# Performance work log

Measured on AMD Instinct MI355X. Metric: run time of the kernel, lower is better.

## Reference

```python
import jax, jax.numpy as jnp
import numpy as np

IN_FEATURES = 4096
OUT_FEATURES = 4096
ALPHA = 0.002
BETA = 0.01


def setup_inputs() -> dict:
    key = jax.random.key(0)
    k_x, k_w, k_b = jax.random.split(key, 3)
    # int8 activations, weights, bias (matching torch.randint(-127, 127, ...))
    x = jax.random.randint(k_x, (4, 2048, IN_FEATURES), -127, 127, dtype=jnp.int32).astype(jnp.int8)
    weight = jax.random.randint(k_w, (OUT_FEATURES, IN_FEATURES), -127, 127, dtype=jnp.int32).astype(jnp.int8)
    bias = jax.random.randint(k_b, (1, OUT_FEATURES), -127, 127, dtype=jnp.int32).astype(jnp.int8)
    a = jnp.float32(ALPHA)
    b = jnp.float32(BETA)
    return {"x": x, "weight": weight, "bias": bias, "a": a, "b": b}


def reference(x, weight, bias, a, b):
    # int8 bias add, and requantize-to-int8 epilogue.
    x_shape = x.shape
    x2d = x.reshape(-1, x_shape[-1])                       # [M, K] int8
    # int32 accumulation: acc = x @ W^T
    acc = jnp.matmul(x2d.astype(jnp.int32), weight.T.astype(jnp.int32),
                     preferred_element_type=jnp.int32)      # [M, N] int32
    # epilogue: alpha * acc + beta * bias, round + clamp to int8 range
    y = a * acc.astype(jnp.float32) + b * bias.astype(jnp.float32)
    y = jnp.clip(jnp.round(y), -128.0, 127.0).astype(jnp.int8)
    return y.reshape(*x_shape[:-1], -1)
```

## Files before the change

### kernel.cpp

```cpp
#include <hip/hip_runtime.h>

#define K_DIM 4096
#define N_DIM 4096
#define NT (K_DIM / 128)

typedef int v4i __attribute__((ext_vector_type(4)));
typedef int v16i __attribute__((ext_vector_type(16)));

__device__ __forceinline__ void gload_lds16(const void* g, void* l) {
  __builtin_amdgcn_global_load_lds(
      (const __attribute__((address_space(1))) void*)g,
      (__attribute__((address_space(3))) void*)l, 16, 0, 0);
}

__device__ __forceinline__ int pack4(int4 w) {
  return (w.x & 0xff) | ((w.y & 0xff) << 8) | ((w.z & 0xff) << 16) | (w.w << 24);
}

__global__ __launch_bounds__(256) void pack_kernel(const int* __restrict__ src,
                                                   int4* __restrict__ dst, int n16) {
  int i = blockIdx.x * 256 + threadIdx.x;
  if (i >= n16) return;
  const int4* s = (const int4*)src + (size_t)i * 4;
  int4 w0 = s[0], w1 = s[1], w2 = s[2], w3 = s[3];
  int4 r;
  r.x = pack4(w0); r.y = pack4(w1); r.z = pack4(w2); r.w = pack4(w3);
  dst[i] = r;
}

__global__ __launch_bounds__(512, 2) void gemm256(
    const char* __restrict__ Ap, const char* __restrict__ Bp,
    const int* __restrict__ bias, const float* __restrict__ pa,
    const float* __restrict__ pb, int* __restrict__ out) {
  extern __shared__ __align__(16) char lds[];

  const int tid = threadIdx.x;
  const int wid = tid >> 6;
  const int lane = tid & 63;

  const int nwg = gridDim.x;
  const int cpx = nwg >> 3;
  const int flat = blockIdx.x;
  const int wg = (flat & 7) * cpx + (flat >> 3);
  const int br = wg >> 4;
  const int bn = wg & 15;

  const int wr = wid >> 2;
  const int wcol = wid & 3;

  const int srow = tid >> 3;
  const int schunk = (tid & 7) ^ (srow & 7);
  const char* aSrc = Ap + (size_t)(br * 256 + srow) * K_DIM + schunk * 16;
  const char* bSrc = Bp + (size_t)(bn * 256 + srow) * K_DIM + schunk * 16;
  char* const dA = lds + tid * 16;
  char* const dB = lds + 65536 + tid * 16;

  auto stage = [&](int kt) {
    const int s = (kt & 1) * 32768;
    const char* sa = aSrc + kt * 128;
    const char* sbp = bSrc + kt * 128;
#pragma unroll
    for (int j = 0; j < 4; ++j) {
      gload_lds16(sa + (size_t)j * 64 * K_DIM, dA + s + j * 8192);
      gload_lds16(sbp + (size_t)j * 64 * K_DIM, dB + s + j * 8192);
    }
  };

  const int lrow = lane & 31;
  const int hi = lane >> 5;
  const int aBase = (wr * 128 + lrow) * 128;
  const int bBase = 65536 + (wcol * 64 + lrow) * 128;
  const int p0 = ((0 + hi) ^ (lrow & 7)) << 4;
  const int p1 = ((2 + hi) ^ (lrow & 7)) << 4;
  const int p2 = ((4 + hi) ^ (lrow & 7)) << 4;
  const int p3 = ((6 + hi) ^ (lrow & 7)) << 4;

  v16i acc[4][2];
  {
    v16i z = {0};
#pragma unroll
    for (int mi = 0; mi < 4; ++mi)
#pragma unroll
      for (int ni = 0; ni < 2; ++ni) acc[mi][ni] = z;
  }

  stage(0);
  asm volatile("s_waitcnt vmcnt(0)" ::: "memory");
  __builtin_amdgcn_s_barrier();

  for (int kt = 0; kt < NT; ++kt) {
    const int sb = (kt & 1) * 32768;
    if (kt + 1 < NT) stage(kt + 1);

    v4i a0[4], b0[2], a1[4], b1[2];
#pragma unroll
    for (int mi = 0; mi < 4; ++mi) a0[mi] = *(const v4i*)&lds[sb + aBase + mi * 4096 + p0];
#pragma unroll
    for (int ni = 0; ni < 2; ++ni) b0[ni] = *(const v4i*)&lds[sb + bBase + ni * 4096 + p0];
#pragma unroll
    for (int mi = 0; mi < 4; ++mi) a1[mi] = *(const v4i*)&lds[sb + aBase + mi * 4096 + p1];
#pragma unroll
    for (int ni = 0; ni < 2; ++ni) b1[ni] = *(const v4i*)&lds[sb + bBase + ni * 4096 + p1];

    asm volatile("s_waitcnt lgkmcnt(6)" ::: "memory");
    __builtin_amdgcn_sched_barrier(0);
    __builtin_amdgcn_s_setprio(1);
#pragma unroll
    for (int mi = 0; mi < 4; ++mi)
#pragma unroll
      for (int ni = 0; ni < 2; ++ni)
        acc[mi][ni] =
            __builtin_amdgcn_mfma_i32_32x32x32_i8(a0[mi], b0[ni], acc[mi][ni], 0, 0, 0);
    __builtin_amdgcn_s_setprio(0);

    asm volatile("s_waitcnt lgkmcnt(0)" ::: "memory");
    __builtin_amdgcn_sched_barrier(0);
    __builtin_amdgcn_s_setprio(1);
#pragma unroll
    for (int mi = 0; mi < 4; ++mi)
#pragma unroll
      for (int ni = 0; ni < 2; ++ni)
        acc[mi][ni] =
            __builtin_amdgcn_mfma_i32_32x32x32_i8(a1[mi], b1[ni], acc[mi][ni], 0, 0, 0);
    __builtin_amdgcn_s_setprio(0);

#pragma unroll
    for (int mi = 0; mi < 4; ++mi) a0[mi] = *(const v4i*)&lds[sb + aBase + mi * 4096 + p2];
#pragma unroll
    for (int ni = 0; ni < 2; ++ni) b0[ni] = *(const v4i*)&lds[sb + bBase + ni * 4096 + p2];
#pragma unroll
    for (int mi = 0; mi < 4; ++mi) a1[mi] = *(const v4i*)&lds[sb + aBase + mi * 4096 + p3];
#pragma unroll
    for (int ni = 0; ni < 2; ++ni) b1[ni] = *(const v4i*)&lds[sb + bBase + ni * 4096 + p3];

    asm volatile("s_waitcnt lgkmcnt(6)" ::: "memory");
    __builtin_amdgcn_sched_barrier(0);
    __builtin_amdgcn_s_setprio(1);
#pragma unroll
    for (int mi = 0; mi < 4; ++mi)
#pragma unroll
      for (int ni = 0; ni < 2; ++ni)
        acc[mi][ni] =
            __builtin_amdgcn_mfma_i32_32x32x32_i8(a0[mi], b0[ni], acc[mi][ni], 0, 0, 0);
    __builtin_amdgcn_s_setprio(0);

    asm volatile("s_waitcnt lgkmcnt(0)" ::: "memory");
    __builtin_amdgcn_sched_barrier(0);
    __builtin_amdgcn_s_setprio(1);
#pragma unroll
    for (int mi = 0; mi < 4; ++mi)
#pragma unroll
      for (int ni = 0; ni < 2; ++ni)
        acc[mi][ni] =
            __builtin_amdgcn_mfma_i32_32x32x32_i8(a1[mi], b1[ni], acc[mi][ni], 0, 0, 0);
    __builtin_amdgcn_s_setprio(0);

    if (kt + 1 < NT) {
      asm volatile("s_waitcnt vmcnt(0)" ::: "memory");
      __builtin_amdgcn_s_barrier();
    }
  }

  const float alpha = *pa;
  const float beta = *pb;
#pragma unroll
  for (int ni = 0; ni < 2; ++ni) {
    const int n = bn * 256 + wcol * 64 + ni * 32 + lrow;
    const float bb = __fmul_rn(beta, (float)bias[n]);
#pragma unroll
    for (int mi = 0; mi < 4; ++mi) {
#pragma unroll
      for (int r = 0; r < 16; ++r) {
        const int row = (r & 3) + 8 * (r >> 2) + 4 * hi;
        const int m = br * 256 + wr * 128 + mi * 32 + row;
        float y = __fadd_rn(__fmul_rn(alpha, (float)acc[mi][ni][r]), bb);
        y = rintf(y);
        y = fminf(127.f, fmaxf(-128.f, y));
        out[(size_t)m * N_DIM + n] = (int)y;
      }
    }
  }
}

extern "C" void kernel_launch(void* const* d_in, const int* in_sizes, int n_in,
                              void* d_out, int out_size, void* d_ws, size_t ws_size,
                              hipStream_t stream) {
  const int* x = (const int*)d_in[0];
  const int* w = (const int*)d_in[1];
  const int* bias = (const int*)d_in[2];
  const float* pa = (const float*)d_in[3];
  const float* pb = (const float*)d_in[4];
  int* out = (int*)d_out;

  const int M = in_sizes[0] / K_DIM;
  const size_t xBytes = (size_t)M * K_DIM;
  const size_t wBytes = (size_t)N_DIM * K_DIM;

  char* xp = (char*)d_ws;
  char* wp = xp + xBytes;
  const int n16x = (int)(xBytes / 16);
  const int n16w = (int)(wBytes / 16);
  pack_kernel<<<(n16x + 255) / 256, 256, 0, stream>>>(x, (int4*)xp, n16x);
  pack_kernel<<<(n16w + 255) / 256, 256, 0, stream>>>(w, (int4*)wp, n16w);

  const int nwg = (M / 256) * (N_DIM / 256);
  hipFuncSetAttribute((const void*)gemm256,
                      hipFuncAttributeMaxDynamicSharedMemorySize, 131072);
  gemm256<<<nwg, 512, 131072, stream>>>(xp, wp, bias, pa, pb, out);
}
```

Before: 197.8 us.

## Switch to 16x16x64 int8 MFMA with split A/B staging and barriers

Replaces the 32x32x32 int8 MFMA tiling with 16x16x64 MFMA over an 8x4 grid of 16x16 accumulator tiles per wave, changing the LDS read pattern and swizzle offsets. The next-tile global-to-LDS prefetch is split into separate A and B halves, issued between MFMA phases. Extra workgroup barriers are placed around each phase to keep waves in lockstep. The intent is to use the higher-throughput MFMA shape and overlap the copies with compute, at the cost of more barriers per K step.

```diff
diff --git a/kernel.cpp b/kernel.cpp
--- a/kernel.cpp
+++ b/kernel.cpp
@@ -5,7 +5,6 @@
 #define NT (K_DIM / 128)
 
 typedef int v4i __attribute__((ext_vector_type(4)));
-typedef int v16i __attribute__((ext_vector_type(16)));
 
 __device__ __forceinline__ void gload_lds16(const void* g, void* l) {
   __builtin_amdgcn_global_load_lds(
@@ -55,125 +54,129 @@
   char* const dA = lds + tid * 16;
   char* const dB = lds + 65536 + tid * 16;
 
-  auto stage = [&](int kt) {
+  auto stageA = [&](int kt) {
     const int s = (kt & 1) * 32768;
     const char* sa = aSrc + kt * 128;
+#pragma unroll
+    for (int j = 0; j < 4; ++j)
+      gload_lds16(sa + (size_t)j * 64 * K_DIM, dA + s + j * 8192);
+  };
+  auto stageB = [&](int kt) {
+    const int s = (kt & 1) * 32768;
     const char* sbp = bSrc + kt * 128;
 #pragma unroll
-    for (int j = 0; j < 4; ++j) {
-      gload_lds16(sa + (size_t)j * 64 * K_DIM, dA + s + j * 8192);
+    for (int j = 0; j < 4; ++j)
       gload_lds16(sbp + (size_t)j * 64 * K_DIM, dB + s + j * 8192);
-    }
   };
 
-  const int lrow = lane & 31;
-  const int hi = lane >> 5;
+  const int lrow = lane & 15;
+  const int g = lane >> 4;
+  const int pos0 = ((g ^ (lrow & 7)) << 4);
+  const int pos1 = pos0 ^ 64;
   const int aBase = (wr * 128 + lrow) * 128;
   const int bBase = 65536 + (wcol * 64 + lrow) * 128;
-  const int p0 = ((0 + hi) ^ (lrow & 7)) << 4;
-  const int p1 = ((2 + hi) ^ (lrow & 7)) << 4;
-  const int p2 = ((4 + hi) ^ (lrow & 7)) << 4;
-  const int p3 = ((6 + hi) ^ (lrow & 7)) << 4;
-
-  v16i acc[4][2];
+
+  v4i acc[8][4];
   {
-    v16i z = {0};
-#pragma unroll
-    for (int mi = 0; mi < 4; ++mi)
-#pragma unroll
-      for (int ni = 0; ni < 2; ++ni) acc[mi][ni] = z;
+    v4i z = {0, 0, 0, 0};
+#pragma unroll
+    for (int mi = 0; mi < 8; ++mi)
+#pragma unroll
+      for (int ni = 0; ni < 4; ++ni) acc[mi][ni] = z;
   }
 
-  stage(0);
+  stageA(0);
+  stageB(0);
   asm volatile("s_waitcnt vmcnt(0)" ::: "memory");
   __builtin_amdgcn_s_barrier();
 
   for (int kt = 0; kt < NT; ++kt) {
-    const int sb = (kt & 1) * 32768;
-    if (kt + 1 < NT) stage(kt + 1);
-
-    v4i a0[4], b0[2], a1[4], b1[2];
-#pragma unroll
-    for (int mi = 0; mi < 4; ++mi) a0[mi] = *(const v4i*)&lds[sb + aBase + mi * 4096 + p0];
-#pragma unroll
-    for (int ni = 0; ni < 2; ++ni) b0[ni] = *(const v4i*)&lds[sb + bBase + ni * 4096 + p0];
-#pragma unroll
-    for (int mi = 0; mi < 4; ++mi) a1[mi] = *(const v4i*)&lds[sb + aBase + mi * 4096 + p1];
-#pragma unroll
-    for (int ni = 0; ni < 2; ++ni) b1[ni] = *(const v4i*)&lds[sb + bBase + ni * 4096 + p1];
-
-    asm volatile("s_waitcnt lgkmcnt(6)" ::: "memory");
-    __builtin_amdgcn_sched_barrier(0);
-    __builtin_amdgcn_s_setprio(1);
-#pragma unroll
-    for (int mi = 0; mi < 4; ++mi)
-#pragma unroll
-      for (int ni = 0; ni < 2; ++ni)
+    const int d = (kt & 1) * 32768;
+    v4i aL[4], aH[4], bb[4];
+
+#pragma unroll
+    for (int mi = 0; mi < 4; ++mi) aL[mi] = *(const v4i*)&lds[d + aBase + mi * 2048 + pos0];
+#pragma unroll
+    for (int ni = 0; ni < 4; ++ni) bb[ni] = *(const v4i*)&lds[d + bBase + ni * 2048 + pos0];
+    if (kt + 1 < NT) stageA(kt + 1);
+    __builtin_amdgcn_s_barrier();
+    asm volatile("s_waitcnt lgkmcnt(0)" ::: "memory");
+    __builtin_amdgcn_sched_barrier(0);
+    __builtin_amdgcn_s_setprio(1);
+#pragma unroll
+    for (int mi = 0; mi < 4; ++mi)
+#pragma unroll
+      for (int ni = 0; ni < 4; ++ni)
         acc[mi][ni] =
-            __builtin_amdgcn_mfma_i32_32x32x32_i8(a0[mi], b0[ni], acc[mi][ni], 0, 0, 0);
-    __builtin_amdgcn_s_setprio(0);
-
-    asm volatile("s_waitcnt lgkmcnt(0)" ::: "memory");
-    __builtin_amdgcn_sched_barrier(0);
-    __builtin_amdgcn_s_setprio(1);
-#pragma unroll
-    for (int mi = 0; mi < 4; ++mi)
-#pragma unroll
-      for (int ni = 0; ni < 2; ++ni)
+            __builtin_amdgcn_mfma_i32_16x16x64_i8(aL[mi], bb[ni], acc[mi][ni], 0, 0, 0);
+    __builtin_amdgcn_s_setprio(0);
+    __builtin_amdgcn_s_barrier();
+
+#pragma unroll
+    for (int mi = 0; mi < 4; ++mi)
+      aH[mi] = *(const v4i*)&lds[d + aBase + (mi + 4) * 2048 + pos0];
+    if (kt + 1 < NT) stageB(kt + 1);
+    __builtin_amdgcn_s_barrier();
+    asm volatile("s_waitcnt lgkmcnt(0)" ::: "memory");
+    __builtin_amdgcn_sched_barrier(0);
+    __builtin_amdgcn_s_setprio(1);
+#pragma unroll
+    for (int mi = 0; mi < 4; ++mi)
+#pragma unroll
+      for (int ni = 0; ni < 4; ++ni)
+        acc[mi + 4][ni] =
+            __builtin_amdgcn_mfma_i32_16x16x64_i8(aH[mi], bb[ni], acc[mi + 4][ni], 0, 0, 0);
+    __builtin_amdgcn_s_setprio(0);
+    __builtin_amdgcn_s_barrier();
+
+#pragma unroll
+    for (int mi = 0; mi < 4; ++mi) aL[mi] = *(const v4i*)&lds[d + aBase + mi * 2048 + pos1];
+#pragma unroll
+    for (int ni = 0; ni < 4; ++ni) bb[ni] = *(const v4i*)&lds[d + bBase + ni * 2048 + pos1];
+    __builtin_amdgcn_s_barrier();
+    asm volatile("s_waitcnt lgkmcnt(0)" ::: "memory");
+    __builtin_amdgcn_sched_barrier(0);
+    __builtin_amdgcn_s_setprio(1);
+#pragma unroll
+    for (int mi = 0; mi < 4; ++mi)
+#pragma unroll
+      for (int ni = 0; ni < 4; ++ni)
         acc[mi][ni] =
-            __builtin_amdgcn_mfma_i32_32x32x32_i8(a1[mi], b1[ni], acc[mi][ni], 0, 0, 0);
-    __builtin_amdgcn_s_setprio(0);
-
-#pragma unroll
-    for (int mi = 0; mi < 4; ++mi) a0[mi] = *(const v4i*)&lds[sb + aBase + mi * 4096 + p2];
-#pragma unroll
-    for (int ni = 0; ni < 2; ++ni) b0[ni] = *(const v4i*)&lds[sb + bBase + ni * 4096 + p2];
-#pragma unroll
-    for (int mi = 0; mi < 4; ++mi) a1[mi] = *(const v4i*)&lds[sb + aBase + mi * 4096 + p3];
-#pragma unroll
-    for (int ni = 0; ni < 2; ++ni) b1[ni] = *(const v4i*)&lds[sb + bBase + ni * 4096 + p3];
-
-    asm volatile("s_waitcnt lgkmcnt(6)" ::: "memory");
-    __builtin_amdgcn_sched_barrier(0);
-    __builtin_amdgcn_s_setprio(1);
-#pragma unroll
-    for (int mi = 0; mi < 4; ++mi)
-#pragma unroll
-      for (int ni = 0; ni < 2; ++ni)
-        acc[mi][ni] =
-            __builtin_amdgcn_mfma_i32_32x32x32_i8(a0[mi], b0[ni], acc[mi][ni], 0, 0, 0);
-    __builtin_amdgcn_s_setprio(0);
-
-    asm volatile("s_waitcnt lgkmcnt(0)" ::: "memory");
-    __builtin_amdgcn_sched_barrier(0);
-    __builtin_amdgcn_s_setprio(1);
-#pragma unroll
-    for (int mi = 0; mi < 4; ++mi)
-#pragma unroll
-      for (int ni = 0; ni < 2; ++ni)
-        acc[mi][ni] =
-            __builtin_amdgcn_mfma_i32_32x32x32_i8(a1[mi], b1[ni], acc[mi][ni], 0, 0, 0);
-    __builtin_amdgcn_s_setprio(0);
-
-    if (kt + 1 < NT) {
-      asm volatile("s_waitcnt vmcnt(0)" ::: "memory");
-      __builtin_amdgcn_s_barrier();
-    }
+            __builtin_amdgcn_mfma_i32_16x16x64_i8(aL[mi], bb[ni], acc[mi][ni], 0, 0, 0);
+    __builtin_amdgcn_s_setprio(0);
+    __builtin_amdgcn_s_barrier();
+
+#pragma unroll
+    for (int mi = 0; mi < 4; ++mi)
+      aH[mi] = *(const v4i*)&lds[d + aBase + (mi + 4) * 2048 + pos1];
+    asm volatile("s_waitcnt vmcnt(0)" ::: "memory");
+    __builtin_amdgcn_s_barrier();
+    asm volatile("s_waitcnt lgkmcnt(0)" ::: "memory");
+    __builtin_amdgcn_sched_barrier(0);
+    __builtin_amdgcn_s_setprio(1);
+#pragma unroll
+    for (int mi = 0; mi < 4; ++mi)
+#pragma unroll
+      for (int ni = 0; ni < 4; ++ni)
+        acc[mi + 4][ni] =
+            __builtin_amdgcn_mfma_i32_16x16x64_i8(aH[mi], bb[ni], acc[mi + 4][ni], 0, 0, 0);
+    __builtin_amdgcn_s_setprio(0);
+    __builtin_amdgcn_s_barrier();
   }
 
   const float alpha = *pa;
   const float beta = *pb;
-#pragma unroll
-  for (int ni = 0; ni < 2; ++ni) {
-    const int n = bn * 256 + wcol * 64 + ni * 32 + lrow;
-    const float bb = __fmul_rn(beta, (float)bias[n]);
-#pragma unroll
-    for (int mi = 0; mi < 4; ++mi) {
-#pragma unroll
-      for (int r = 0; r < 16; ++r) {
-        const int row = (r & 3) + 8 * (r >> 2) + 4 * hi;
-        const int m = br * 256 + wr * 128 + mi * 32 + row;
-        float y = __fadd_rn(__fmul_rn(alpha, (float)acc[mi][ni][r]), bb);
+  const int rg = lane >> 4;
+#pragma unroll
+  for (int ni = 0; ni < 4; ++ni) {
+    const int n = bn * 256 + wcol * 64 + ni * 16 + lrow;
+    const float bb2 = __fmul_rn(beta, (float)bias[n]);
+#pragma unroll
+    for (int mi = 0; mi < 8; ++mi) {
+#pragma unroll
+      for (int j = 0; j < 4; ++j) {
+        const int m = br * 256 + wr * 128 + mi * 16 + rg * 4 + j;
+        float y = __fadd_rn(__fmul_rn(alpha, (float)acc[mi][ni][j]), bb2);
         y = rintf(y);
         y = fminf(127.f, fmaxf(-128.f, y));
         out[(size_t)m * N_DIM + n] = (int)y;
```

Measured after the change: 191.2 us. 3.4% less time.
